# Performance work log

Measured on AMD Instinct MI355X. Metric: run time of the kernel, lower is better.

Reference implementation:

```python
import jax, jax.numpy as jnp
import numpy as np

INPUT_DIM = 512
OUTPUT_DIM = 512
NUM_BASIS = 16
GRID_MIN, GRID_MAX = -2.0, 2.0
LN_EPS = 1e-5


def rbf_basis(x):
    # x: [batch, input_dim] -> [batch, input_dim, num_basis]
    centers = jnp.linspace(GRID_MIN, GRID_MAX, NUM_BASIS, dtype=x.dtype)  # [K]
    h = (GRID_MAX - GRID_MIN) / (NUM_BASIS - 1)
    z = (x[..., None] - centers) / h
    return jnp.exp(-(z * z))


def setup_inputs() -> dict:
    key = jax.random.key(0)
    k1, k2, k3 = jax.random.split(key, 3)
    x = jax.random.normal(k1, (4096, INPUT_DIM), dtype=jnp.float32)
    weights = jax.random.normal(k2, (OUTPUT_DIM, INPUT_DIM, NUM_BASIS), dtype=jnp.float32) * 0.1
    base_weights = jax.random.normal(k3, (OUTPUT_DIM, INPUT_DIM), dtype=jnp.float32) * 0.1
    ln_gamma = jnp.ones((OUTPUT_DIM,), dtype=jnp.float32)
    ln_beta = jnp.zeros((OUTPUT_DIM,), dtype=jnp.float32)
    return {"x": x, "weights": weights, "base_weights": base_weights,
            "ln_gamma": ln_gamma, "ln_beta": ln_beta}


def reference(x, weights, base_weights, ln_gamma, ln_beta):
    # per-edge basis expansion: [B, I, K]
    basis = rbf_basis(x)
    # fused contraction replacing the nested python loops:
    # out[b, j] = sum_{i,k} basis[b, i, k] * weights[j, i, k]
    out = jnp.einsum('bik,jik->bj', basis, weights)
    # residual base activation path
    out = out + jax.nn.silu(x) @ base_weights.T
    # layer norm over output_dim
    mean = jnp.mean(out, axis=-1, keepdims=True)
    var = jnp.var(out, axis=-1, keepdims=True)
    out = (out - mean) * jax.lax.rsqrt(var + LN_EPS) * ln_gamma + ln_beta
    return out
```

## Files before the change

### kernel.cpp

```cpp
#include <hip/hip_runtime.h>
#include <hip/hip_bf16.h>


typedef __bf16 bf16x8 __attribute__((ext_vector_type(8)));
typedef __bf16 bf16x4 __attribute__((ext_vector_type(4)));
typedef float  f32x4  __attribute__((ext_vector_type(4)));

#define KT 8704
#define SPLITS 4
#define KS (KT / SPLITS)
#define CP_STRIDE (4096 * 512)

__device__ __forceinline__ void gll16(const __bf16* g, __bf16* l) {
    __builtin_amdgcn_global_load_lds(
        (const __attribute__((address_space(1))) void*)g,
        (__attribute__((address_space(3))) void*)l, 16, 0, 0);
}

__global__ void prep_A(const float* __restrict__ x, __bf16* __restrict__ A) {
    int t = blockIdx.x * 256 + threadIdx.x;
    int b = t >> 9;
    int i = t & 511;
    float xv = x[t];
    float zb = 3.75f * xv + 7.5f;
    bf16x8 lo, hi;
#pragma unroll
    for (int k = 0; k < 8; ++k) { float z = zb - (float)k;     lo[k]   = (__bf16)__expf(-z * z); }
#pragma unroll
    for (int k = 8; k < 16; ++k){ float z = zb - (float)k;     hi[k-8] = (__bf16)__expf(-z * z); }
    size_t base = (size_t)b * KT + (size_t)i * 16;
    *(bf16x8*)(A + base)     = lo;
    *(bf16x8*)(A + base + 8) = hi;
    float s = xv / (1.0f + __expf(-xv));
    A[(size_t)b * KT + 8192 + i] = (__bf16)s;
}

__global__ void prep_B(const float* __restrict__ W, const float* __restrict__ Wb,
                       __bf16* __restrict__ B) {
    int t = blockIdx.x * 256 + threadIdx.x;
    int j  = t / 2176;
    int c  = (t - j * 2176) * 4;
    float4 v;
    if (c < 8192) v = *(const float4*)&W[(size_t)j * 8192 + c];
    else          v = *(const float4*)&Wb[(size_t)j * 512 + (c - 8192)];
    bf16x4 o;
    o[0] = (__bf16)v.x; o[1] = (__bf16)v.y; o[2] = (__bf16)v.z; o[3] = (__bf16)v.w;
    *(bf16x4*)&B[(size_t)j * KT + c] = o;
}

__global__ __launch_bounds__(256, 2) void gemm_bt(const __bf16* __restrict__ A,
                                                  const __bf16* __restrict__ B,
                                                  float* __restrict__ Cp) {
    __shared__ __attribute__((aligned(16))) __bf16 As[128 * 32];
    __shared__ __attribute__((aligned(16))) __bf16 Bs[128 * 32];

    const int tid  = threadIdx.x;
    const int wave = tid >> 6, lane = tid & 63;
    const int q    = lane >> 4, r16 = lane & 15;
    const int m0 = blockIdx.x * 128, n0 = blockIdx.y * 128, k0 = blockIdx.z * KS;
    const int wm = wave & 1, wn = wave >> 1;

    const __bf16* gA0 = A + (size_t)(m0 + (tid >> 2)) * KT + k0 + (tid & 3) * 8;
    const __bf16* gA1 = gA0 + (size_t)64 * KT;
    const __bf16* gB0 = B + (size_t)(n0 + (tid >> 2)) * KT + k0 + (tid & 3) * 8;
    const __bf16* gB1 = gB0 + (size_t)64 * KT;
    __bf16* lA0 = &As[tid * 8];
    __bf16* lA1 = &As[(tid + 256) * 8];
    __bf16* lB0 = &Bs[tid * 8];
    __bf16* lB1 = &Bs[(tid + 256) * 8];

    f32x4 acc[4][4] = {};

    const __bf16* Aw = &As[(wm * 64 + r16) * 32 + q * 8];
    const __bf16* Bw = &Bs[(wn * 64 + r16) * 32 + q * 8];

    for (int it = 0; it < KS / 32; ++it) {
        const int ko = it * 32;
        gll16(gA0 + ko, lA0);
        gll16(gA1 + ko, lA1);
        gll16(gB0 + ko, lB0);
        gll16(gB1 + ko, lB1);
        __syncthreads();

        bf16x8 af[4], bg[4];
#pragma unroll
        for (int mi = 0; mi < 4; ++mi) af[mi] = *(const bf16x8*)(Aw + mi * 512);
#pragma unroll
        for (int ni = 0; ni < 4; ++ni) bg[ni] = *(const bf16x8*)(Bw + ni * 512);
#pragma unroll
        for (int mi = 0; mi < 4; ++mi)
#pragma unroll
            for (int ni = 0; ni < 4; ++ni)
                acc[mi][ni] = __builtin_amdgcn_mfma_f32_16x16x32_bf16(
                    af[mi], bg[ni], acc[mi][ni], 0, 0, 0);
        __syncthreads();
    }

    float* Cb = Cp + (size_t)blockIdx.z * CP_STRIDE;
#pragma unroll
    for (int mi = 0; mi < 4; ++mi) {
        const int row = m0 + wm * 64 + mi * 16 + q * 4;
#pragma unroll
        for (int ni = 0; ni < 4; ++ni) {
            const int col = n0 + wn * 64 + ni * 16 + r16;
#pragma unroll
            for (int r = 0; r < 4; ++r)
                Cb[(size_t)(row + r) * 512 + col] = acc[mi][ni][r];
        }
    }
}

__global__ void ln_kernel(const float* __restrict__ Cp, const float* __restrict__ gamma,
                          const float* __restrict__ beta, float* __restrict__ out) {
    const int tid  = threadIdx.x;
    const int wave = tid >> 6, lane = tid & 63;
    const int row  = blockIdx.x * 4 + wave;
    const float* p = Cp + (size_t)row * 512;
    float v[8], s = 0.f, s2 = 0.f;
#pragma unroll
    for (int u = 0; u < 8; ++u) {
        const int col = lane + u * 64;
        float a = p[col] + p[col + CP_STRIDE] + p[col + 2 * CP_STRIDE] + p[col + 3 * CP_STRIDE];
        v[u] = a; s += a; s2 += a * a;
    }
#pragma unroll
    for (int m = 32; m >= 1; m >>= 1) {
        s  += __shfl_xor(s, m);
        s2 += __shfl_xor(s2, m);
    }
    const float mean = s * (1.0f / 512.0f);
    const float var  = s2 * (1.0f / 512.0f) - mean * mean;
    const float rs   = rsqrtf(var + 1e-5f);
#pragma unroll
    for (int u = 0; u < 8; ++u) {
        const int col = lane + u * 64;
        out[(size_t)row * 512 + col] = (v[u] - mean) * rs * gamma[col] + beta[col];
    }
}

extern "C" void kernel_launch(void* const* d_in, const int* in_sizes, int n_in,
                              void* d_out, int out_size, void* d_ws, size_t ws_size,
                              hipStream_t stream) {
    const float* x     = (const float*)d_in[0];
    const float* W     = (const float*)d_in[1];
    const float* Wb    = (const float*)d_in[2];
    const float* gamma = (const float*)d_in[3];
    const float* beta  = (const float*)d_in[4];
    float* out = (float*)d_out;

    char* ws = (char*)d_ws;
    __bf16* A  = (__bf16*)ws;
    __bf16* Bm = (__bf16*)(ws + 71303168);
    float*  Cp = (float*)(ws + 71303168 + 8912896);

    prep_A<<<8192, 256, 0, stream>>>(x, A);
    prep_B<<<4352, 256, 0, stream>>>(W, Wb, Bm);
    dim3 g(32, 4, SPLITS);
    gemm_bt<<<g, 256, 0, stream>>>(A, Bm, Cp);
    ln_kernel<<<1024, 256, 0, stream>>>(Cp, gamma, beta, out);
}
```

Before: 151.7 us.

## Merge prep kernels, swizzle LDS, double split-K, store bf16 partials

Merges the A and B prep kernels into one launch. Adds an XOR swizzle to the LDS layout to cut bank conflicts on the MFMA fragment reads. Doubles split-K to 8, raises the launch-bounds occupancy hint to 4, and writes partial sums as bf16 instead of fp32. The layernorm kernel now reads bf16x8 and writes float4, to reduce partial-sum traffic. Rounding each partial to bf16 costs accuracy in the pre-norm sums.

```diff
diff --git a/kernel.cpp b/kernel.cpp
--- a/kernel.cpp
+++ b/kernel.cpp
@@ -7,9 +7,9 @@
 typedef float  f32x4  __attribute__((ext_vector_type(4)));
 
 #define KT 8704
-#define SPLITS 4
+#define SPLITS 8
 #define KS (KT / SPLITS)
-#define CP_STRIDE (4096 * 512)
+#define CPE (4096 * 512)
 
 __device__ __forceinline__ void gll16(const __bf16* g, __bf16* l) {
     __builtin_amdgcn_global_load_lds(
@@ -17,40 +17,41 @@
         (__attribute__((address_space(3))) void*)l, 16, 0, 0);
 }
 
-__global__ void prep_A(const float* __restrict__ x, __bf16* __restrict__ A) {
-    int t = blockIdx.x * 256 + threadIdx.x;
-    int b = t >> 9;
-    int i = t & 511;
-    float xv = x[t];
-    float zb = 3.75f * xv + 7.5f;
-    bf16x8 lo, hi;
+__global__ void prep_AB(const float* __restrict__ x, const float* __restrict__ W,
+                        const float* __restrict__ Wb, __bf16* __restrict__ A,
+                        __bf16* __restrict__ B) {
+    if (blockIdx.x < 8192) {
+        int t = blockIdx.x * 256 + threadIdx.x;
+        int b = t >> 9;
+        int i = t & 511;
+        float xv = x[t];
+        float zb = 3.75f * xv + 7.5f;
+        bf16x8 lo, hi;
 #pragma unroll
-    for (int k = 0; k < 8; ++k) { float z = zb - (float)k;     lo[k]   = (__bf16)__expf(-z * z); }
+        for (int k = 0; k < 8; ++k) { float z = zb - (float)k; lo[k]   = (__bf16)__expf(-z * z); }
 #pragma unroll
-    for (int k = 8; k < 16; ++k){ float z = zb - (float)k;     hi[k-8] = (__bf16)__expf(-z * z); }
-    size_t base = (size_t)b * KT + (size_t)i * 16;
-    *(bf16x8*)(A + base)     = lo;
-    *(bf16x8*)(A + base + 8) = hi;
-    float s = xv / (1.0f + __expf(-xv));
-    A[(size_t)b * KT + 8192 + i] = (__bf16)s;
+        for (int k = 8; k < 16; ++k){ float z = zb - (float)k; hi[k-8] = (__bf16)__expf(-z * z); }
+        size_t base = (size_t)b * KT + (size_t)i * 16;
+        *(bf16x8*)(A + base)     = lo;
+        *(bf16x8*)(A + base + 8) = hi;
+        float s = xv / (1.0f + __expf(-xv));
+        A[(size_t)b * KT + 8192 + i] = (__bf16)s;
+    } else {
+        int t = (blockIdx.x - 8192) * 256 + threadIdx.x;
+        int j = t / 2176;
+        int c = (t - j * 2176) * 4;
+        float4 v;
+        if (c < 8192) v = *(const float4*)&W[(size_t)j * 8192 + c];
+        else          v = *(const float4*)&Wb[(size_t)j * 512 + (c - 8192)];
+        bf16x4 o;
+        o[0] = (__bf16)v.x; o[1] = (__bf16)v.y; o[2] = (__bf16)v.z; o[3] = (__bf16)v.w;
+        *(bf16x4*)&B[(size_t)j * KT + c] = o;
+    }
 }
 
-__global__ void prep_B(const float* __restrict__ W, const float* __restrict__ Wb,
-                       __bf16* __restrict__ B) {
-    int t = blockIdx.x * 256 + threadIdx.x;
-    int j  = t / 2176;
-    int c  = (t - j * 2176) * 4;
-    float4 v;
-    if (c < 8192) v = *(const float4*)&W[(size_t)j * 8192 + c];
-    else          v = *(const float4*)&Wb[(size_t)j * 512 + (c - 8192)];
-    bf16x4 o;
-    o[0] = (__bf16)v.x; o[1] = (__bf16)v.y; o[2] = (__bf16)v.z; o[3] = (__bf16)v.w;
-    *(bf16x4*)&B[(size_t)j * KT + c] = o;
-}
-
-__global__ __launch_bounds__(256, 2) void gemm_bt(const __bf16* __restrict__ A,
+__global__ __launch_bounds__(256, 4) void gemm_bt(const __bf16* __restrict__ A,
                                                   const __bf16* __restrict__ B,
-                                                  float* __restrict__ Cp) {
+                                                  __bf16* __restrict__ Cp) {
     __shared__ __attribute__((aligned(16))) __bf16 As[128 * 32];
     __shared__ __attribute__((aligned(16))) __bf16 Bs[128 * 32];
 
@@ -60,10 +61,12 @@
     const int m0 = blockIdx.x * 128, n0 = blockIdx.y * 128, k0 = blockIdx.z * KS;
     const int wm = wave & 1, wn = wave >> 1;
 
-    const __bf16* gA0 = A + (size_t)(m0 + (tid >> 2)) * KT + k0 + (tid & 3) * 8;
-    const __bf16* gA1 = gA0 + (size_t)64 * KT;
-    const __bf16* gB0 = B + (size_t)(n0 + (tid >> 2)) * KT + k0 + (tid & 3) * 8;
-    const __bf16* gB1 = gB0 + (size_t)64 * KT;
+    const int row0 = tid >> 2, qk0 = (tid & 3) ^ ((row0 >> 1) & 3);
+    const int row1 = row0 + 64, qk1 = (tid & 3) ^ ((row1 >> 1) & 3);
+    const __bf16* gA0 = A + (size_t)(m0 + row0) * KT + k0 + qk0 * 8;
+    const __bf16* gA1 = A + (size_t)(m0 + row1) * KT + k0 + qk1 * 8;
+    const __bf16* gB0 = B + (size_t)(n0 + row0) * KT + k0 + qk0 * 8;
+    const __bf16* gB1 = B + (size_t)(n0 + row1) * KT + k0 + qk1 * 8;
     __bf16* lA0 = &As[tid * 8];
     __bf16* lA1 = &As[(tid + 256) * 8];
     __bf16* lB0 = &Bs[tid * 8];
@@ -71,8 +74,9 @@
 
     f32x4 acc[4][4] = {};
 
-    const __bf16* Aw = &As[(wm * 64 + r16) * 32 + q * 8];
-    const __bf16* Bw = &Bs[(wn * 64 + r16) * 32 + q * 8];
+    const int qa = q ^ ((r16 >> 1) & 3);
+    const __bf16* Aw = &As[(wm * 64 + r16) * 32 + qa * 8];
+    const __bf16* Bw = &Bs[(wn * 64 + r16) * 32 + qa * 8];
 
     for (int it = 0; it < KS / 32; ++it) {
         const int ko = it * 32;
@@ -96,7 +100,7 @@
         __syncthreads();
     }
 
-    float* Cb = Cp + (size_t)blockIdx.z * CP_STRIDE;
+    __bf16* Cb = Cp + (size_t)blockIdx.z * CPE;
 #pragma unroll
     for (int mi = 0; mi < 4; ++mi) {
         const int row = m0 + wm * 64 + mi * 16 + q * 4;
@@ -105,24 +109,28 @@
             const int col = n0 + wn * 64 + ni * 16 + r16;
 #pragma unroll
             for (int r = 0; r < 4; ++r)
-                Cb[(size_t)(row + r) * 512 + col] = acc[mi][ni][r];
+                Cb[(size_t)(row + r) * 512 + col] = (__bf16)acc[mi][ni][r];
         }
     }
 }
 
-__global__ void ln_kernel(const float* __restrict__ Cp, const float* __restrict__ gamma,
+__global__ void ln_kernel(const __bf16* __restrict__ Cp, const float* __restrict__ gamma,
                           const float* __restrict__ beta, float* __restrict__ out) {
     const int tid  = threadIdx.x;
     const int wave = tid >> 6, lane = tid & 63;
     const int row  = blockIdx.x * 4 + wave;
-    const float* p = Cp + (size_t)row * 512;
-    float v[8], s = 0.f, s2 = 0.f;
+    const size_t base = (size_t)row * 512 + lane * 8;
+
+    float v[8] = {};
+    float s = 0.f, s2 = 0.f;
 #pragma unroll
-    for (int u = 0; u < 8; ++u) {
-        const int col = lane + u * 64;
-        float a = p[col] + p[col + CP_STRIDE] + p[col + 2 * CP_STRIDE] + p[col + 3 * CP_STRIDE];
-        v[u] = a; s += a; s2 += a * a;
+    for (int z = 0; z < SPLITS; ++z) {
+        bf16x8 p = *(const bf16x8*)(Cp + (size_t)z * CPE + base);
+#pragma unroll
+        for (int j = 0; j < 8; ++j) v[j] += (float)p[j];
     }
+#pragma unroll
+    for (int j = 0; j < 8; ++j) { s += v[j]; s2 += v[j] * v[j]; }
 #pragma unroll
     for (int m = 32; m >= 1; m >>= 1) {
         s  += __shfl_xor(s, m);
@@ -131,11 +139,21 @@
     const float mean = s * (1.0f / 512.0f);
     const float var  = s2 * (1.0f / 512.0f) - mean * mean;
     const float rs   = rsqrtf(var + 1e-5f);
-#pragma unroll
-    for (int u = 0; u < 8; ++u) {
-        const int col = lane + u * 64;
-        out[(size_t)row * 512 + col] = (v[u] - mean) * rs * gamma[col] + beta[col];
-    }
+    float4 o0, o1;
+    const float4 g0 = *(const float4*)&gamma[lane * 8];
+    const float4 g1 = *(const float4*)&gamma[lane * 8 + 4];
+    const float4 b0 = *(const float4*)&beta[lane * 8];
+    const float4 b1 = *(const float4*)&beta[lane * 8 + 4];
+    o0.x = (v[0] - mean) * rs * g0.x + b0.x;
+    o0.y = (v[1] - mean) * rs * g0.y + b0.y;
+    o0.z = (v[2] - mean) * rs * g0.z + b0.z;
+    o0.w = (v[3] - mean) * rs * g0.w + b0.w;
+    o1.x = (v[4] - mean) * rs * g1.x + b1.x;
+    o1.y = (v[5] - mean) * rs * g1.y + b1.y;
+    o1.z = (v[6] - mean) * rs * g1.z + b1.z;
+    o1.w = (v[7] - mean) * rs * g1.w + b1.w;
+    *(float4*)&out[base]     = o0;
+    *(float4*)&out[base + 4] = o1;
 }
 
 extern "C" void kernel_launch(void* const* d_in, const int* in_sizes, int n_in,
@@ -151,10 +169,9 @@
     char* ws = (char*)d_ws;
     __bf16* A  = (__bf16*)ws;
     __bf16* Bm = (__bf16*)(ws + 71303168);
-    float*  Cp = (float*)(ws + 71303168 + 8912896);
+    __bf16* Cp = (__bf16*)(ws + 80216064);
 
-    prep_A<<<8192, 256, 0, stream>>>(x, A);
-    prep_B<<<4352, 256, 0, stream>>>(W, Wb, Bm);
+    prep_AB<<<8192 + 4352, 256, 0, stream>>>(x, W, Wb, A, Bm);
     dim3 g(32, 4, SPLITS);
     gemm_bt<<<g, 256, 0, stream>>>(A, Bm, Cp);
     ln_kernel<<<1024, 256, 0, stream>>>(Cp, gamma, beta, out);
```

Result: no change. 148.9 us (-1.8%).
